# Kernel tuning notes

Measured on AMD Instinct MI355X. Metric: run time of the kernel, lower is better.

Reference implementation:

```python
import math
import jax, jax.numpy as jnp
import numpy as np

HIDDEN = 1024
HEADS = 16
HEAD_DIM = HIDDEN // HEADS  # 64
SEQ = 4096
PATCH = 4064  # num rotated (patch) tokens; last PATCH positions get RoPE
EPS = 1e-6


def setup_inputs() -> dict:
    key = jax.random.key(0)
    ks = jax.random.split(key, 8)
    return {
        "x": jax.random.normal(ks[0], (1, SEQ, HIDDEN), dtype=jnp.float32),
        "rope_cos": jax.random.uniform(ks[1], (PATCH, HEAD_DIM // 2), dtype=jnp.float32),
        "rope_sin": jax.random.uniform(ks[2], (PATCH, HEAD_DIM // 2), dtype=jnp.float32),
        "wq": jax.random.normal(ks[3], (HIDDEN, HIDDEN), dtype=jnp.float32) / math.sqrt(HIDDEN),
        "wk": jax.random.normal(ks[4], (HIDDEN, HIDDEN), dtype=jnp.float32) / math.sqrt(HIDDEN),
        "wv": jax.random.normal(ks[5], (HIDDEN, HIDDEN), dtype=jnp.float32) / math.sqrt(HIDDEN),
        "wo": jax.random.normal(ks[6], (HIDDEN, HIDDEN), dtype=jnp.float32) / math.sqrt(HIDDEN),
        "q_norm_w": jnp.ones((HEAD_DIM,), dtype=jnp.float32),
        "k_norm_w": jnp.ones((HEAD_DIM,), dtype=jnp.float32),
    }


def _rms_norm(t, w):
    # RMSNorm over the last (head_dim) axis
    return t * jax.lax.rsqrt(jnp.mean(t * t, axis=-1, keepdims=True) + EPS) * w


def _apply_rope(t, cos, sin):
    # t: [b, s, h, d]; rotate only the last PATCH positions, pairwise complex mul
    b, s, h, d = t.shape
    P = cos.shape[0]
    tail = t[:, s - P:].reshape(b, P, h, d // 2, 2)
    x0, x1 = tail[..., 0], tail[..., 1]
    c = cos[None, :, None, :]
    sn = sin[None, :, None, :]
    rot = jnp.stack([x0 * c - x1 * sn, x0 * sn + x1 * c], axis=-1).reshape(b, P, h, d)
    return jnp.concatenate([t[:, : s - P], rot], axis=1)


def reference(x, rope_cos, rope_sin, wq, wk, wv, wo, q_norm_w, k_norm_w):
    b, s, _ = x.shape
    q = (x @ wq.T).reshape(b, s, HEADS, HEAD_DIM)
    k = (x @ wk.T).reshape(b, s, HEADS, HEAD_DIM)
    v = (x @ wv.T).reshape(b, s, HEADS, HEAD_DIM)
    q = _rms_norm(q, q_norm_w)
    k = _rms_norm(k, k_norm_w)
    q = _apply_rope(q, rope_cos, rope_sin)
    k = _apply_rope(k, rope_cos, rope_sin)
    q = q / math.sqrt(HEAD_DIM)
    scores = jnp.einsum('bqhd,bkhd->bhqk', q, k)
    attn = jax.nn.softmax(scores.astype(jnp.float32), axis=-1)
    out = jnp.einsum('bhqk,bkhd->bqhd', attn, v).reshape(b, s, HIDDEN)
    return out @ wo.T
```

## Files before the change

kernel.cpp:

```cpp
#include <hip/hip_runtime.h>
#include <hip/hip_bf16.h>
#include <stdint.h>

#define HIDDEN 1024
#define HEADS 16
#define HEAD_DIM 64
#define SEQ 4096
#define PATCH 4064
#define SKIP 32

typedef __attribute__((ext_vector_type(8))) short bf16x8;
typedef __attribute__((ext_vector_type(4))) float f32x4;
typedef __attribute__((ext_vector_type(2))) float f32x2;
typedef __attribute__((ext_vector_type(16))) float f32x16;

__device__ __forceinline__ float b2f(unsigned short u){
  union{uint32_t i; float f;} c; c.i = ((uint32_t)u)<<16; return c.f;
}
__device__ __forceinline__ unsigned short f2b(float f){
  union{float f; uint32_t i;} c; c.f=f;
  uint32_t r = c.i + 0x7fffu + ((c.i>>16)&1u);
  return (unsigned short)(r>>16);
}
__device__ __forceinline__ uint32_t cvtpk(float a, float b){
  uint32_t r;
  asm("v_cvt_pk_bf16_f32 %0, %1, %2" : "=v"(r) : "v"(a), "v"(b));
  return r;
}

#define GLD16(gp, lp) __builtin_amdgcn_global_load_lds( \
    (const __attribute__((address_space(1))) void*)(gp), \
    (__attribute__((address_space(3))) void*)(lp), 16, 0, 0)

__global__ __launch_bounds__(256) void convert_all(
    const float* __restrict__ x,  const float* __restrict__ wq,
    const float* __restrict__ wk, const float* __restrict__ wv,
    const float* __restrict__ wo,
    unsigned short* __restrict__ xb,  unsigned short* __restrict__ wqb,
    unsigned short* __restrict__ wkb, unsigned short* __restrict__ wvb,
    unsigned short* __restrict__ wob)
{
  size_t u = (size_t)blockIdx.x*256 + threadIdx.x;
  size_t e = u*8;
  const float* src; unsigned short* dst; size_t off;
  if      (e < 4194304ull) { src=x;  dst=xb;  off=e;            }
  else if (e < 5242880ull) { src=wq; dst=wqb; off=e-4194304ull; }
  else if (e < 6291456ull) { src=wk; dst=wkb; off=e-5242880ull; }
  else if (e < 7340032ull) { src=wv; dst=wvb; off=e-6291456ull; }
  else                     { src=wo; dst=wob; off=e-7340032ull; }
  float4 v0 = *(const float4*)(src+off);
  float4 v1 = *(const float4*)(src+off+4);
  union { bf16x8 v; unsigned short h[8]; } o;
  o.h[0]=f2b(v0.x); o.h[1]=f2b(v0.y); o.h[2]=f2b(v0.z); o.h[3]=f2b(v0.w);
  o.h[4]=f2b(v1.x); o.h[5]=f2b(v1.y); o.h[6]=f2b(v1.z); o.h[7]=f2b(v1.w);
  *(bf16x8*)(dst+off) = o.v;
}

template<int OUT_BF16>
__global__ __launch_bounds__(256) void gemm_bt(
    const unsigned short* __restrict__ A,
    const unsigned short* __restrict__ B0,
    const unsigned short* __restrict__ B1,
    const unsigned short* __restrict__ B2,
    float* __restrict__ Cf, unsigned short* __restrict__ Cb,
    int M, int Nper, int K)
{
  __shared__ unsigned short As[128*32];
  __shared__ unsigned short Bs[128*32];
  const int tid = threadIdx.x;
  const int w = tid>>6, l = tid&63;
  const int wm = w>>1, wn = w&1;
  const int g = l>>4, lr = l&15;
  const int bm = blockIdx.x;
  int bn = blockIdx.y;
  const int tilesPer = Nper >> 7;
  const int sel = bn / tilesPer;
  bn -= sel*tilesPer;
  const unsigned short* Bsel = (sel==0) ? B0 : ((sel==1) ? B1 : B2);
  const size_t outBase = (size_t)sel * (size_t)M * (size_t)Nper;

  const int off0 = w*1024 + l*16;
  const int r0 = off0>>6, c0 = (off0&63)>>1;
  const int off1 = off0 + 4096;
  const int r1 = off1>>6, c1 = (off1&63)>>1;

  const unsigned short* Ab = A    + (size_t)(bm*128)*K;
  const unsigned short* Bb = Bsel + (size_t)(bn*128)*K;

  f32x4 zero = {0.f,0.f,0.f,0.f};
  f32x4 acc[4][4];
  #pragma unroll
  for (int m=0;m<4;m++)
    #pragma unroll
    for (int n=0;n<4;n++) acc[m][n]=zero;

  for (int kt = 0; kt < K; kt += 32) {
    GLD16(Ab + (size_t)r0*K + kt + c0, (char*)As + off0);
    GLD16(Ab + (size_t)r1*K + kt + c1, (char*)As + off1);
    GLD16(Bb + (size_t)r0*K + kt + c0, (char*)Bs + off0);
    GLD16(Bb + (size_t)r1*K + kt + c1, (char*)Bs + off1);
    __syncthreads();
    bf16x8 a[4], b[4];
    #pragma unroll
    for (int m=0;m<4;m++)
      a[m] = *(const bf16x8*)&As[(wm*64 + m*16 + lr)*32 + g*8];
    #pragma unroll
    for (int n=0;n<4;n++)
      b[n] = *(const bf16x8*)&Bs[(wn*64 + n*16 + lr)*32 + g*8];
    #pragma unroll
    for (int m=0;m<4;m++)
      #pragma unroll
      for (int n=0;n<4;n++)
        acc[m][n] = __builtin_amdgcn_mfma_f32_16x16x32_bf16(a[m], b[n], acc[m][n], 0,0,0);
    __syncthreads();
  }
  #pragma unroll
  for (int m=0;m<4;m++){
    const int row = bm*128 + wm*64 + m*16 + g*4;
    #pragma unroll
    for (int n=0;n<4;n++){
      const int col = bn*128 + wn*64 + n*16 + lr;
      #pragma unroll
      for (int r=0;r<4;r++){
        if (OUT_BF16) Cb[outBase + (size_t)(row+r)*Nper + col] = f2b(acc[m][n][r]);
        else          Cf[outBase + (size_t)(row+r)*Nper + col] = acc[m][n][r];
      }
    }
  }
}

__global__ __launch_bounds__(256) void prep_qk(
    unsigned short* __restrict__ q, unsigned short* __restrict__ k,
    const float* __restrict__ rc, const float* __restrict__ rs,
    const float* __restrict__ qw, const float* __restrict__ kw)
{
  const int gw   = (blockIdx.x*256 + threadIdx.x) >> 6;
  const int lane = threadIdx.x & 63;
  const int s = gw >> 4, h = gw & 15;
  const size_t base = (size_t)s*HIDDEN + h*HEAD_DIM + lane;
  const bool rope = (s >= SKIP);
  float c = 1.f, sn = 0.f;
  if (rope) {
    const int p = s - SKIP;
    c  = rc[p*(HEAD_DIM/2) + (lane>>1)];
    sn = rs[p*(HEAD_DIM/2) + (lane>>1)];
  }
  {
    float v = b2f(q[base]);
    float ss = v*v;
    #pragma unroll
    for (int off=1; off<64; off<<=1) ss += __shfl_xor(ss, off);
    const float rn = rsqrtf(ss*(1.f/64.f) + 1e-6f);
    v = v * rn * qw[lane];
    if (rope) {
      const float partner = __shfl_xor(v, 1);
      v = (lane&1) ? (partner*sn + v*c) : (v*c - partner*sn);
    }
    q[base] = f2b(v * 0.18033688011112042f);
  }
  {
    float v = b2f(k[base]);
    float ss = v*v;
    #pragma unroll
    for (int off=1; off<64; off<<=1) ss += __shfl_xor(ss, off);
    const float rn = rsqrtf(ss*(1.f/64.f) + 1e-6f);
    v = v * rn * kw[lane];
    if (rope) {
      const float partner = __shfl_xor(v, 1);
      v = (lane&1) ? (partner*sn + v*c) : (v*c - partner*sn);
    }
    k[base] = f2b(v);
  }
}

__global__ __launch_bounds__(256) void transpose_v(
    const unsigned short* __restrict__ v, unsigned short* __restrict__ vt)
{
  __shared__ unsigned short t[64*72];
  const int h = blockIdx.y;
  const int s0 = blockIdx.x * 64;
  const int tid = threadIdx.x;
  #pragma unroll
  for (int i=0;i<2;i++){
    const int e = tid + i*256;
    const int r = e>>3, cc = (e&7)*8;
    *(bf16x8*)&t[r*72+cc] = *(const bf16x8*)(v + (size_t)(s0+r)*HIDDEN + h*HEAD_DIM + cc);
  }
  __syncthreads();
  #pragma unroll
  for (int i=0;i<2;i++){
    const int e = tid + i*256;
    const int d = e>>3, sc = (e&7)*8;
    union { bf16x8 v8; unsigned short h8[8]; } o;
    #pragma unroll
    for (int j=0;j<8;j++){
      const int x  = sc + j;
      const int px = (x & ~12) | ((x&4)<<1) | ((x&8)>>1);
      o.h8[j] = t[px*72 + d];
    }
    *(bf16x8*)(vt + (size_t)(h*HEAD_DIM + d)*SEQ + s0 + sc) = o.v8;
  }
}

__global__ __launch_bounds__(256, 4) void attn_kernel(
    const unsigned short* __restrict__ q, const unsigned short* __restrict__ k,
    const unsigned short* __restrict__ vt, unsigned short* __restrict__ po,
    float* __restrict__ lbuf)
{
  __shared__ unsigned short smem[16384];
  const int h    = blockIdx.y;
  const int q0   = blockIdx.x * 128;
  const int half = blockIdx.z;
  const int tid = threadIdx.x;
  const int w = tid>>6, l = tid&63;
  const int hi = l>>5, lo = l&31;
  const int NT = SEQ/64/2;
  const int tbase = half * NT;

  const int cA = tid, cB = tid + 256;
  const int rA = cA>>3, rB = cB>>3;
  const int colA = ((cA&7)*16) ^ ((rA&7)<<4);
  const int colB = ((cB&7)*16) ^ ((rB&7)<<4);
  const unsigned short* kA = k  + (size_t)rA*HIDDEN + h*HEAD_DIM + (colA>>1);
  const unsigned short* kB = k  + (size_t)rB*HIDDEN + h*HEAD_DIM + (colB>>1);
  const unsigned short* vA = vt + ((size_t)(h*HEAD_DIM + rA))*SEQ + (colA>>1);
  const unsigned short* vB = vt + ((size_t)(h*HEAD_DIM + rB))*SEQ + (colB>>1);

#define STAGE(b, kOffE, vOffE) do { \
    GLD16(kA + (kOffE), (char*)smem + (b)*16384 + cA*16); \
    GLD16(kB + (kOffE), (char*)smem + (b)*16384 + cB*16); \
    GLD16(vA + (vOffE), (char*)smem + (b)*16384 + 8192 + cA*16); \
    GLD16(vB + (vOffE), (char*)smem + (b)*16384 + 8192 + cB*16); \
  } while(0)

  const int swz = (lo&7)<<4;
  int colo[4];
  #pragma unroll
  for (int ks=0; ks<4; ks++) colo[ks] = ((2*ks+hi)*16) ^ swz;

  bf16x8 qf[4];
  {
    const unsigned short* qp = q + (size_t)(q0 + w*32 + lo)*HIDDEN + h*HEAD_DIM;
    #pragma unroll
    for (int ks=0; ks<4; ks++)
      qf[ks] = *(const bf16x8*)(qp + ks*16 + hi*8);
  }

  f32x16 ot[2];
  #pragma unroll
  for (int m2=0;m2<2;m2++)
    #pragma unroll
    for (int i=0;i<16;i++) ot[m2][i] = 0.f;
  f32x2 lacc = {0.f, 0.f};

  STAGE(0, (size_t)tbase*64*HIDDEN, (size_t)tbase*64);

  for (int t = 0; t < NT; ++t) {
    const int buf = t & 1;
    __syncthreads();
    if (t+1 < NT) {
      const size_t ta = (size_t)(tbase + t + 1);
      STAGE((t+1)&1, ta*64*HIDDEN, ta*64);
    }

    const char* Kb = (const char*)smem + buf*16384;
    const char* Vb = Kb + 8192;

    f32x16 st[2];
    __builtin_amdgcn_s_setprio(1);
    #pragma unroll
    for (int c=0;c<2;c++){
      #pragma unroll
      for (int i=0;i<16;i++) st[c][i] = 0.f;
      #pragma unroll
      for (int ks=0; ks<4; ks++){
        bf16x8 a = *(const bf16x8*)(Kb + (32*c+lo)*128 + colo[ks]);
        st[c] = __builtin_amdgcn_mfma_f32_32x32x16_bf16(a, qf[ks], st[c], 0,0,0);
      }
    }
    __builtin_amdgcn_s_setprio(0);

    #pragma unroll
    for (int c=0;c<2;c++)
      #pragma unroll
      for (int i=0;i<16;i++) st[c][i] = __builtin_amdgcn_exp2f(st[c][i]);

    #pragma unroll
    for (int c=0;c<2;c++)
      #pragma unroll
      for (int i=0;i<8;i++){
        f32x2 a; a.x = st[c][2*i]; a.y = st[c][2*i+1];
        lacc += a;
      }

    bf16x8 pf[4];
    #pragma unroll
    for (int t2=0; t2<2; t2++)
      #pragma unroll
      for (int e=0; e<2; e++){
        union { uint32_t u4[4]; bf16x8 v8; } pu;
        #pragma unroll
        for (int u=0; u<4; u++)
          pu.u4[u] = cvtpk(st[t2][e*8+2*u], st[t2][e*8+2*u+1]);
        pf[2*t2+e] = pu.v8;
      }

    __builtin_amdgcn_s_setprio(1);
    #pragma unroll
    for (int m2=0;m2<2;m2++)
      #pragma unroll
      for (int ks=0; ks<4; ks++){
        bf16x8 a = *(const bf16x8*)(Vb + (32*m2+lo)*128 + colo[ks]);
        ot[m2] = __builtin_amdgcn_mfma_f32_32x32x16_bf16(a, pf[ks], ot[m2], 0,0,0);
      }
    __builtin_amdgcn_s_setprio(0);
  }

  float ls = lacc.x + lacc.y;
  ls += __shfl_xor(ls, 32);
  if (hi == 0)
    lbuf[(size_t)half*HEADS*SEQ + h*SEQ + q0 + w*32 + lo] = ls;

  unsigned short* pout = po + (size_t)half*SEQ*HIDDEN;
  #pragma unroll
  for (int m2=0;m2<2;m2++)
    #pragma unroll
    for (int f=0; f<4; f++)
      #pragma unroll
      for (int u=0; u<2; u++){
        const uint32_t wrd = cvtpk(ot[m2][4*f+2*u], ot[m2][4*f+2*u+1]);
        const int d = 32*m2 + 8*f + 4*hi + 2*u;
        *(uint32_t*)((char*)smem + (w*32+lo)*128 + ((d*2) ^ swz)) = wrd;
      }
  __syncthreads();
  {
    const int ql = tid>>1, xh = tid&1;
    #pragma unroll
    for (int i=0;i<4;i++){
      const int cb = xh*64 + i*16;
      bf16x8 vv = *(const bf16x8*)((const char*)smem + ql*128 + (cb ^ ((ql&7)<<4)));
      *(bf16x8*)(pout + (size_t)(q0+ql)*HIDDEN + h*HEAD_DIM + (cb>>1)) = vv;
    }
  }
#undef STAGE
}

__global__ __launch_bounds__(256) void combine_halves(
    const unsigned short* __restrict__ po, const float* __restrict__ lbuf,
    unsigned short* __restrict__ at)
{
  const size_t e = ((size_t)blockIdx.x*256 + threadIdx.x)*8;
  const int qrow = (int)(e >> 10);
  const int h = (int)((e >> 6) & 15);
  const float li = 1.0f / (lbuf[h*SEQ + qrow] + lbuf[HEADS*SEQ + h*SEQ + qrow]);
  union { bf16x8 v; unsigned short s[8]; } a, b, o;
  a.v = *(const bf16x8*)(po + e);
  b.v = *(const bf16x8*)(po + (size_t)SEQ*HIDDEN + e);
  #pragma unroll
  for (int j=0;j<8;j++)
    o.s[j] = f2b((b2f(a.s[j]) + b2f(b.s[j])) * li);
  *(bf16x8*)(at + e) = o.v;
}

extern "C" void kernel_launch(void* const* d_in, const int* in_sizes, int n_in,
                              void* d_out, int out_size, void* d_ws, size_t ws_size,
                              hipStream_t stream)
{
  const float* x  = (const float*)d_in[0];
  const float* rc = (const float*)d_in[1];
  const float* rs = (const float*)d_in[2];
  const float* wq = (const float*)d_in[3];
  const float* wk = (const float*)d_in[4];
  const float* wv = (const float*)d_in[5];
  const float* wo = (const float*)d_in[6];
  const float* qw = (const float*)d_in[7];
  const float* kw = (const float*)d_in[8];
  float* out = (float*)d_out;

  char* ws = (char*)d_ws;
  const size_t MB = 1024*1024;
  unsigned short* xb  = (unsigned short*)(ws + 0);
  unsigned short* wqb = (unsigned short*)(ws + 8*MB);
  unsigned short* wkb = (unsigned short*)(ws + 10*MB);
  unsigned short* wvb = (unsigned short*)(ws + 12*MB);
  unsigned short* wob = (unsigned short*)(ws + 14*MB);
  unsigned short* qkv = (unsigned short*)(ws + 16*MB);
  unsigned short* qb = qkv;
  unsigned short* kb = qkv + (size_t)SEQ*HIDDEN;
  unsigned short* vb = qkv + (size_t)2*SEQ*HIDDEN;
  unsigned short* vt = (unsigned short*)(ws + 0);
  float*          lbuf = (float*)(ws + 8*MB);
  unsigned short* po = (unsigned short*)(ws + 32*MB);
  unsigned short* at = (unsigned short*)(ws + 40*MB);

  convert_all<<<4096, 256, 0, stream>>>(x, wq, wk, wv, wo, xb, wqb, wkb, wvb, wob);
  gemm_bt<1><<<dim3(32,24), 256, 0, stream>>>(xb, wqb, wkb, wvb, nullptr, qkv, SEQ, HIDDEN, HIDDEN);
  prep_qk<<<16384, 256, 0, stream>>>(qb, kb, rc, rs, qw, kw);
  transpose_v<<<dim3(64,16), 256, 0, stream>>>(vb, vt);
  attn_kernel<<<dim3(32,16,2), 256, 0, stream>>>(qb, kb, vt, po, lbuf);
  combine_halves<<<2048, 256, 0, stream>>>(po, lbuf, at);
  gemm_bt<0><<<dim3(32,8), 256, 0, stream>>>(at, wob, wob, wob, out, nullptr, SEQ, HIDDEN, HIDDEN);
}
```

Baseline: 183.0 us.

## Fuse QK RMSNorm+RoPE into QKV GEMM epilogue; split-K the output projection

```diff
diff --git a/kernel.cpp b/kernel.cpp
--- a/kernel.cpp
+++ b/kernel.cpp
@@ -56,14 +56,18 @@
   *(bf16x8*)(dst+off) = o.v;
 }
 
-template<int OUT_BF16>
+template<int MODE>
 __global__ __launch_bounds__(256) void gemm_bt(
     const unsigned short* __restrict__ A,
     const unsigned short* __restrict__ B0,
     const unsigned short* __restrict__ B1,
     const unsigned short* __restrict__ B2,
-    float* __restrict__ Cf, unsigned short* __restrict__ Cb,
-    int M, int Nper, int K)
+    float* __restrict__ Cf,
+    unsigned short* __restrict__ qout, unsigned short* __restrict__ kout,
+    unsigned short* __restrict__ vout,
+    const float* __restrict__ rc, const float* __restrict__ rs,
+    const float* __restrict__ qw, const float* __restrict__ kw,
+    int M, int Nper, int K, int kSpan)
 {
   __shared__ unsigned short As[128*32];
   __shared__ unsigned short Bs[128*32];
@@ -77,7 +81,8 @@
   const int sel = bn / tilesPer;
   bn -= sel*tilesPer;
   const unsigned short* Bsel = (sel==0) ? B0 : ((sel==1) ? B1 : B2);
-  const size_t outBase = (size_t)sel * (size_t)M * (size_t)Nper;
+  const int kStart = blockIdx.z * kSpan;
+  const int kEnd = kStart + kSpan;
 
   const int off0 = w*1024 + l*16;
   const int r0 = off0>>6, c0 = (off0&63)>>1;
@@ -94,7 +99,7 @@
     #pragma unroll
     for (int n=0;n<4;n++) acc[m][n]=zero;
 
-  for (int kt = 0; kt < K; kt += 32) {
+  for (int kt = kStart; kt < kEnd; kt += 32) {
     GLD16(Ab + (size_t)r0*K + kt + c0, (char*)As + off0);
     GLD16(Ab + (size_t)r1*K + kt + c1, (char*)As + off1);
     GLD16(Bb + (size_t)r0*K + kt + c0, (char*)Bs + off0);
@@ -114,62 +119,73 @@
         acc[m][n] = __builtin_amdgcn_mfma_f32_16x16x32_bf16(a[m], b[n], acc[m][n], 0,0,0);
     __syncthreads();
   }
-  #pragma unroll
-  for (int m=0;m<4;m++){
-    const int row = bm*128 + wm*64 + m*16 + g*4;
-    #pragma unroll
-    for (int n=0;n<4;n++){
-      const int col = bn*128 + wn*64 + n*16 + lr;
-      #pragma unroll
-      for (int r=0;r<4;r++){
-        if (OUT_BF16) Cb[outBase + (size_t)(row+r)*Nper + col] = f2b(acc[m][n][r]);
-        else          Cf[outBase + (size_t)(row+r)*Nper + col] = acc[m][n][r];
-      }
-    }
-  }
-}
-
-__global__ __launch_bounds__(256) void prep_qk(
-    unsigned short* __restrict__ q, unsigned short* __restrict__ k,
-    const float* __restrict__ rc, const float* __restrict__ rs,
-    const float* __restrict__ qw, const float* __restrict__ kw)
-{
-  const int gw   = (blockIdx.x*256 + threadIdx.x) >> 6;
-  const int lane = threadIdx.x & 63;
-  const int s = gw >> 4, h = gw & 15;
-  const size_t base = (size_t)s*HIDDEN + h*HEAD_DIM + lane;
-  const bool rope = (s >= SKIP);
-  float c = 1.f, sn = 0.f;
-  if (rope) {
-    const int p = s - SKIP;
-    c  = rc[p*(HEAD_DIM/2) + (lane>>1)];
-    sn = rs[p*(HEAD_DIM/2) + (lane>>1)];
-  }
-  {
-    float v = b2f(q[base]);
-    float ss = v*v;
-    #pragma unroll
-    for (int off=1; off<64; off<<=1) ss += __shfl_xor(ss, off);
-    const float rn = rsqrtf(ss*(1.f/64.f) + 1e-6f);
-    v = v * rn * qw[lane];
-    if (rope) {
-      const float partner = __shfl_xor(v, 1);
-      v = (lane&1) ? (partner*sn + v*c) : (v*c - partner*sn);
-    }
-    q[base] = f2b(v * 0.18033688011112042f);
-  }
-  {
-    float v = b2f(k[base]);
-    float ss = v*v;
-    #pragma unroll
-    for (int off=1; off<64; off<<=1) ss += __shfl_xor(ss, off);
-    const float rn = rsqrtf(ss*(1.f/64.f) + 1e-6f);
-    v = v * rn * kw[lane];
-    if (rope) {
-      const float partner = __shfl_xor(v, 1);
-      v = (lane&1) ? (partner*sn + v*c) : (v*c - partner*sn);
-    }
-    k[base] = f2b(v);
+
+  if constexpr (MODE == 0) {
+    #pragma unroll
+    for (int m=0;m<4;m++){
+      const int row = bm*128 + wm*64 + m*16 + g*4;
+      #pragma unroll
+      for (int n=0;n<4;n++){
+        const int col = bn*128 + wn*64 + n*16 + lr;
+        #pragma unroll
+        for (int r=0;r<4;r++)
+          atomicAdd(&Cf[(size_t)(row+r)*Nper + col], acc[m][n][r]);
+      }
+    }
+  } else {
+    if (sel <= 1) {
+      const float* nw = (sel==0) ? qw : kw;
+      unsigned short* dst = (sel==0) ? qout : kout;
+      const float scl = (sel==0) ? 0.18033688011112042f : 1.0f;
+      float wl[4];
+      #pragma unroll
+      for (int n=0;n<4;n++) wl[n] = nw[n*16+lr];
+      const int hglob = bn*2 + wn;
+      #pragma unroll
+      for (int m=0;m<4;m++){
+        const int rowb = bm*128 + wm*64 + m*16 + g*4;
+        float rn[4];
+        #pragma unroll
+        for (int r=0;r<4;r++){
+          float ss = 0.f;
+          #pragma unroll
+          for (int n=0;n<4;n++) ss += acc[m][n][r]*acc[m][n][r];
+          ss += __shfl_xor(ss,1); ss += __shfl_xor(ss,2);
+          ss += __shfl_xor(ss,4); ss += __shfl_xor(ss,8);
+          rn[r] = rsqrtf(ss*(1.f/64.f) + 1e-6f);
+        }
+        #pragma unroll
+        for (int r=0;r<4;r++){
+          const int row = rowb + r;
+          const int p = row - SKIP;
+          #pragma unroll
+          for (int n=0;n<4;n++){
+            float v = acc[m][n][r]*rn[r]*wl[n];
+            float c = 1.f, sn = 0.f;
+            if (p >= 0){
+              const int d2 = (n*16+lr)>>1;
+              c  = rc[p*(HEAD_DIM/2) + d2];
+              sn = rs[p*(HEAD_DIM/2) + d2];
+            }
+            const float partner = __shfl_xor(v, 1);
+            const float o2 = (lr&1) ? (partner*sn + v*c) : (v*c - partner*sn);
+            dst[(size_t)row*HIDDEN + hglob*64 + n*16 + lr] = f2b(o2*scl);
+          }
+        }
+      }
+    } else {
+      #pragma unroll
+      for (int m=0;m<4;m++){
+        const int row = bm*128 + wm*64 + m*16 + g*4;
+        #pragma unroll
+        for (int n=0;n<4;n++){
+          const int col = bn*128 + wn*64 + n*16 + lr;
+          #pragma unroll
+          for (int r=0;r<4;r++)
+            vout[(size_t)(row+r)*HIDDEN + col] = f2b(acc[m][n][r]);
+        }
+      }
+    }
   }
 }
 
@@ -394,10 +410,14 @@
   unsigned short* at = (unsigned short*)(ws + 40*MB);
 
   convert_all<<<4096, 256, 0, stream>>>(x, wq, wk, wv, wo, xb, wqb, wkb, wvb, wob);
-  gemm_bt<1><<<dim3(32,24), 256, 0, stream>>>(xb, wqb, wkb, wvb, nullptr, qkv, SEQ, HIDDEN, HIDDEN);
-  prep_qk<<<16384, 256, 0, stream>>>(qb, kb, rc, rs, qw, kw);
+  gemm_bt<1><<<dim3(32,24,1), 256, 0, stream>>>(
+      xb, wqb, wkb, wvb, nullptr, qb, kb, vb, rc, rs, qw, kw,
+      SEQ, HIDDEN, HIDDEN, HIDDEN);
   transpose_v<<<dim3(64,16), 256, 0, stream>>>(vb, vt);
   attn_kernel<<<dim3(32,16,2), 256, 0, stream>>>(qb, kb, vt, po, lbuf);
   combine_halves<<<2048, 256, 0, stream>>>(po, lbuf, at);
-  gemm_bt<0><<<dim3(32,8), 256, 0, stream>>>(at, wob, wob, wob, out, nullptr, SEQ, HIDDEN, HIDDEN);
-}
+  hipMemsetAsync(out, 0, (size_t)out_size*sizeof(float), stream);
+  gemm_bt<0><<<dim3(32,8,2), 256, 0, stream>>>(
+      at, wob, wob, wob, out, nullptr, nullptr, nullptr, nullptr, nullptr, nullptr, nullptr,
+      SEQ, HIDDEN, HIDDEN, HIDDEN/2);
+}
```

Result: slower. 193.3 us (+5.7%).
